# Kernel optimization log

Measured on AMD Instinct MI355X. Metric: run time of the kernel, lower is better.

The kernel has to match this reference:

```python
import jax, jax.numpy as jnp
import numpy as np
import math

B, L, E, H, D = 2, 2048, 2048, 16, 128
LOGIT_SCALE_MAX = math.log(1.0 / 0.01)
EPS = 1e-6


def rms_norm(x, scale, eps=EPS):
    # UIOLayerNorm: no mean subtraction, no bias, fp32 internals
    x32 = x.astype(jnp.float32)
    ms = jnp.mean(x32 * x32, axis=-1, keepdims=True)
    return (scale * (x32 * jax.lax.rsqrt(ms + eps)).astype(x.dtype)).astype(x.dtype)


def apply_rotary(x, rope):
    # x: [b, l, h, d]; rope: [b, l, d] interpreted as (cos, sin) interleaved pairs
    b, l, h, d = x.shape
    xr = x.astype(jnp.float32).reshape(b, l, h, d // 2, 2)
    rc = rope.astype(jnp.float32).reshape(b, l, 1, d // 2, 2)
    out = jnp.stack(
        [xr[..., 0] * rc[..., 0] - xr[..., 1] * rc[..., 1],
         xr[..., 1] * rc[..., 0] + xr[..., 0] * rc[..., 1]], axis=-1)
    return out.reshape(b, l, h, d).astype(x.dtype)


def l2_normalize(x, eps=1e-12):
    # matches F.normalize(dim=-1): x / max(||x||, eps)
    n = jnp.sqrt(jnp.sum(x * x, axis=-1, keepdims=True))
    return x / jnp.maximum(n, eps)


def setup_inputs() -> dict:
    key = jax.random.key(0)
    ks = jax.random.split(key, 12)
    scale = 1.0 / math.sqrt(E)
    return {
        "inputs_q": jax.random.normal(ks[0], (B, L, E), jnp.float32),
        "inputs_kv": jax.random.normal(ks[1], (B, L, E), jnp.float32),
        "bias": jax.random.normal(ks[2], (1, 1, L, L), jnp.float32),
        "q_sinusoids": jax.random.uniform(ks[3], (B, L, D), jnp.float32, -1.0, 1.0),
        "k_sinusoids": jax.random.uniform(ks[4], (B, L, D), jnp.float32, -1.0, 1.0),
        "Wq": jax.random.normal(ks[5], (E, E), jnp.float32) * scale,
        "Wk": jax.random.normal(ks[6], (E, E), jnp.float32) * scale,
        "Wv": jax.random.normal(ks[7], (E, E), jnp.float32) * scale,
        "Wo": jax.random.normal(ks[8], (E, E), jnp.float32) * scale,
        "q_norm_scale": jnp.ones((D,), jnp.float32),
        "k_norm_scale": jnp.ones((D,), jnp.float32),
        "logit_scale": jnp.full((H,), math.log(10.0), jnp.float32),
    }


def reference(inputs_q, inputs_kv, bias, q_sinusoids, k_sinusoids,
              Wq, Wk, Wv, Wo, q_norm_scale, k_norm_scale, logit_scale):
    dtype = inputs_q.dtype
    b, ql, e = inputs_q.shape
    kl = inputs_kv.shape[1]
    # QKV projections (nn.Linear, no bias), split heads -> [b, len, h, d]
    q = (inputs_q @ Wq.T).reshape(b, ql, H, D)
    k = (inputs_kv @ Wk.T).reshape(b, kl, H, D)
    v = (inputs_kv @ Wv.T).reshape(b, kl, H, D)
    # qk_norm (UIO RMS norm over head_dim)
    q = rms_norm(q, q_norm_scale)
    k = rms_norm(k, k_norm_scale)
    # RoPE
    q = apply_rotary(q, q_sinusoids)
    k = apply_rotary(k, k_sinusoids)
    # float32_logits
    q32 = q.astype(jnp.float32)
    k32 = k.astype(jnp.float32)
    # scaled cosine attention: L2-normalize q,k; learned per-head logit scale
    scores = jnp.einsum("bqhd,bkhd->bhqk", l2_normalize(q32), l2_normalize(k32))
    ls = jnp.exp(jnp.minimum(logit_scale, LOGIT_SCALE_MAX))
    scores = scores * ls[None, :, None, None]
    scores = scores + bias.astype(scores.dtype)
    attn = jax.nn.softmax(scores, axis=-1).astype(dtype)
    out = jnp.einsum("bhqk,bkhd->bqhd", attn, v)
    out = out.reshape(b, ql, e)
    return out @ Wo.T
```

## Files before the change

kernel.cpp:

```cpp
#include <hip/hip_runtime.h>
#include <hip/hip_bf16.h>

#define B_ 2
#define L_ 2048
#define E_ 2048
#define H_ 16
#define D_ 128
#define M_ (B_*L_)
#define NT_ (E_/64)
#define LOGIT_SCALE_MAX_ 4.6051701859880914f
#define LOG2E_ 1.44269504088896f

typedef __bf16 bf16_t;
typedef __bf16 bf16x2 __attribute__((ext_vector_type(2)));
typedef __bf16 bf16x4 __attribute__((ext_vector_type(4)));
typedef __bf16 bf16x8 __attribute__((ext_vector_type(8)));
typedef float f32x4 __attribute__((ext_vector_type(4)));
typedef float f32x16 __attribute__((ext_vector_type(16)));

#define KS_BYTE(r, cb) ((r) * 256 + ((cb) ^ (((r) & 7) << 4)))
#define VS_BYTE(r, cb) (16384 + (r) * 128 + ((cb) ^ (((r) & 7) << 4)))

#define GEMM_FRAG_IDX(r, kk, fq) ((r) * 64 + ((((kk) * 4 + (fq)) ^ ((r) & 7)) * 8))

#define NW_ 4194304L
#define NX_ 8388608L
__global__ void cvt_all_k(const float* __restrict__ xq, const float* __restrict__ xkv,
                          const float* __restrict__ bias,
                          const float* __restrict__ wq, const float* __restrict__ wk,
                          const float* __restrict__ wv, const float* __restrict__ wo,
                          bf16_t* __restrict__ ws) {
    const long NW4 = NW_ / 4, NX4 = NX_ / 4;
    long i4 = (long)blockIdx.x * 256 + threadIdx.x;
    const float* src; long off; float scale = 1.0f;
    if (i4 < 4 * NW4) {
        long r = i4 / NW4;
        src = (r == 0) ? wq : (r == 1) ? wk : (r == 2) ? wv : wo;
        off = i4 - r * NW4;
    } else if (i4 < 5 * NW4) {
        src = bias; off = i4 - 4 * NW4; scale = LOG2E_;
    } else if (i4 < 5 * NW4 + NX4) {
        src = xq; off = i4 - 5 * NW4;
    } else {
        src = xkv; off = i4 - 5 * NW4 - NX4;
    }
    float4 v = ((const float4*)src)[off];
    bf16x4 o = { (bf16_t)(v.x * scale), (bf16_t)(v.y * scale),
                 (bf16_t)(v.z * scale), (bf16_t)(v.w * scale) };
    ((bf16x4*)ws)[i4] = o;
}

template<typename OutT, int GROUPS>
__global__ __launch_bounds__(256, 2) void gemm_pipe(
    const bf16_t* __restrict__ A0, const bf16_t* __restrict__ A1,
    const bf16_t* __restrict__ W0, OutT* __restrict__ C0) {
    __shared__ bf16_t As[2][128 * 64];
    __shared__ bf16_t Bs[2][128 * 64];
    const int tid = threadIdx.x;
    const int wid = tid >> 6, lane = tid & 63;
    int bid = blockIdx.x;
    {
        int cpx = (int)gridDim.x >> 3;
        bid = (bid & 7) * cpx + (bid >> 3);
    }
    const int g = bid >> 9;
    const int wg = bid & 511;
    const int bm = wg >> 4, bn = wg & 15;
    const long arow0 = (long)bm * 128;
    const long brow0 = (long)bn * 128;
    const int fr = lane & 15, fq = lane >> 4;
    const int srow = lane >> 3;
    const int scol = ((lane & 7) ^ srow) * 8;
    const int wm = wid >> 1, wn = wid & 1;
    const bf16_t* Ab = ((GROUPS > 1 && g > 0) ? A1 : A0) + arow0 * E_;
    const bf16_t* Wb = W0 + (long)g * E_ * E_ + brow0 * E_;
    OutT* Cg = C0 + (long)g * M_ * E_;

    f32x4 acc[4][4] = {};

    auto STAGE = [&](int kt, int p) {
        #pragma unroll
        for (int q = 0; q < 4; ++q) {
            int row = wid * 32 + q * 8 + srow;
            __builtin_amdgcn_global_load_lds(
                (const __attribute__((address_space(1))) void*)(Ab + (long)row * E_ + kt + scol),
                (__attribute__((address_space(3))) void*)(&As[p][(wid * 32 + q * 8) * 64]), 16, 0, 0);
            __builtin_amdgcn_global_load_lds(
                (const __attribute__((address_space(1))) void*)(Wb + (long)row * E_ + kt + scol),
                (__attribute__((address_space(3))) void*)(&Bs[p][(wid * 32 + q * 8) * 64]), 16, 0, 0);
        }
    };

    STAGE(0, 0);
    int p = 0;
    bf16x8 a[2][4], b[2][4];
    for (int t = 0; t < NT_ - 1; ++t) {
        STAGE((t + 1) * 64, p ^ 1);
        asm volatile("s_waitcnt vmcnt(8)" ::: "memory");
        __builtin_amdgcn_s_barrier();
        __builtin_amdgcn_sched_barrier(0);
        #pragma unroll
        for (int kk = 0; kk < 2; ++kk) {
            #pragma unroll
            for (int mi = 0; mi < 4; ++mi)
                a[kk][mi] = *(const bf16x8*)&As[p][GEMM_FRAG_IDX(wm * 64 + mi * 16 + fr, kk, fq)];
            #pragma unroll
            for (int ni = 0; ni < 4; ++ni)
                b[kk][ni] = *(const bf16x8*)&Bs[p][GEMM_FRAG_IDX(wn * 64 + ni * 16 + fr, kk, fq)];
        }
        asm volatile("s_waitcnt lgkmcnt(0)" ::: "memory");
        __builtin_amdgcn_sched_barrier(0);
        __builtin_amdgcn_s_barrier();
        __builtin_amdgcn_s_setprio(1);
        #pragma unroll
        for (int kk = 0; kk < 2; ++kk)
            #pragma unroll
            for (int mi = 0; mi < 4; ++mi)
                #pragma unroll
                for (int ni = 0; ni < 4; ++ni)
                    acc[mi][ni] = __builtin_amdgcn_mfma_f32_16x16x32_bf16(a[kk][mi], b[kk][ni], acc[mi][ni], 0, 0, 0);
        __builtin_amdgcn_s_setprio(0);
        p ^= 1;
    }
    asm volatile("s_waitcnt vmcnt(0)" ::: "memory");
    __builtin_amdgcn_s_barrier();
    __builtin_amdgcn_sched_barrier(0);
    #pragma unroll
    for (int kk = 0; kk < 2; ++kk) {
        #pragma unroll
        for (int mi = 0; mi < 4; ++mi)
            a[kk][mi] = *(const bf16x8*)&As[p][GEMM_FRAG_IDX(wm * 64 + mi * 16 + fr, kk, fq)];
        #pragma unroll
        for (int ni = 0; ni < 4; ++ni)
            b[kk][ni] = *(const bf16x8*)&Bs[p][GEMM_FRAG_IDX(wn * 64 + ni * 16 + fr, kk, fq)];
        #pragma unroll
        for (int mi = 0; mi < 4; ++mi)
            #pragma unroll
            for (int ni = 0; ni < 4; ++ni)
                acc[mi][ni] = __builtin_amdgcn_mfma_f32_16x16x32_bf16(a[kk][mi], b[kk][ni], acc[mi][ni], 0, 0, 0);
    }
    #pragma unroll
    for (int mi = 0; mi < 4; ++mi) {
        #pragma unroll
        for (int i = 0; i < 4; ++i) {
            long row = arow0 + wm * 64 + mi * 16 + fq * 4 + i;
            OutT* crow = Cg + row * E_ + brow0 + wn * 64 + fr;
            #pragma unroll
            for (int ni = 0; ni < 4; ++ni)
                crow[ni * 16] = (OutT)acc[mi][ni][i];
        }
    }
}

__global__ __launch_bounds__(256) void postproc_k(
    const bf16_t* __restrict__ Pq, const bf16_t* __restrict__ Pk,
    const float* __restrict__ qsins, const float* __restrict__ ksins,
    const float* __restrict__ qnscale, const float* __restrict__ knscale,
    bf16_t* __restrict__ outq, bf16_t* __restrict__ outk) {
    const int wid = threadIdx.x >> 6, lane = threadIdx.x & 63;
    const int half = blockIdx.x >> 14;
    const long g = (long)(blockIdx.x & 16383) * 4 + wid;
    const bf16_t* P = half ? Pk : Pq;
    const float* sins = half ? ksins : qsins;
    const float* nscale = half ? knscale : qnscale;
    bf16_t* out = half ? outk : outq;
    const int h = (int)(g % H_);
    const long bl = g / H_;
    const int b = (int)(bl / L_), l = (int)(bl % L_);
    bf16x2 xv = *(const bf16x2*)(P + g * D_ + lane * 2);
    float x0 = (float)xv[0], x1 = (float)xv[1];
    float ss = x0 * x0 + x1 * x1;
    #pragma unroll
    for (int m = 1; m < 64; m <<= 1) ss += __shfl_xor(ss, m);
    float r = rsqrtf(ss * (1.0f / 128.0f) + 1e-6f);
    float y0 = x0 * r * nscale[lane * 2];
    float y1 = x1 * r * nscale[lane * 2 + 1];
    float2 cs = *(const float2*)(sins + bl * D_ + lane * 2);
    float z0 = y0 * cs.x - y1 * cs.y;
    float z1 = y1 * cs.x + y0 * cs.y;
    float n2 = z0 * z0 + z1 * z1;
    #pragma unroll
    for (int m = 1; m < 64; m <<= 1) n2 += __shfl_xor(n2, m);
    float inv = 1.0f / fmaxf(sqrtf(n2), 1e-12f);
    bf16x2 o = { (bf16_t)(z0 * inv), (bf16_t)(z1 * inv) };
    *(bf16x2*)(out + (((long)b * H_ + h) * L_ + l) * D_ + lane * 2) = o;
}

__global__ __launch_bounds__(256) void transpose_v_k(
    const bf16_t* __restrict__ Vp, bf16_t* __restrict__ Vt) {
    __shared__ bf16_t t[64 * 64];
    const int lb = blockIdx.x;
    const int db = blockIdx.y;
    const int bh = blockIdx.z;
    const int b = bh >> 4, h = bh & 15;
    const bf16_t* src = Vp + ((long)(b * L_ + lb * 64) * H_ + h) * D_ + db * 64;
    #pragma unroll
    for (int it = 0; it < 2; ++it) {
        int i = it * 256 + threadIdx.x;
        int r = i >> 3, c8 = i & 7;
        bf16x8 v = *(const bf16x8*)(src + (long)r * H_ * D_ + c8 * 8);
        *(bf16x8*)&t[r * 64 + (c8 ^ (r >> 3)) * 8] = v;
    }
    __syncthreads();
    bf16_t* dst = Vt + ((long)(b * H_ + h) * D_ + db * 64) * L_ + lb * 64;
    #pragma unroll
    for (int it = 0; it < 2; ++it) {
        int i = it * 256 + threadIdx.x;
        int d = i >> 3, l8 = i & 7;
        bf16x8 o;
        #pragma unroll
        for (int j = 0; j < 8; ++j) {
            int l = l8 * 8 + j;
            o[j] = t[l * 64 + ((d >> 3) ^ l8) * 8 + (d & 7)];
        }
        *(bf16x8*)(dst + (long)d * L_ + l8 * 8) = o;
    }
}

__global__ __launch_bounds__(256, 2) void attn_k(
    const bf16_t* __restrict__ Qn, const bf16_t* __restrict__ Kn,
    const bf16_t* __restrict__ Vt, const bf16_t* __restrict__ biasb,
    const float* __restrict__ lsg, bf16_t* __restrict__ AO) {
    __shared__ __align__(16) unsigned char smem[34816];
    const int tid = threadIdx.x;
    const int w = tid >> 6, lane = tid & 63;
    const int lane31 = lane & 31, hi = lane >> 5;
    const int qb = blockIdx.x, bh = blockIdx.y;
    const int b = bh >> 4, h = bh & 15;
    const float lsc2 = __expf(fminf(lsg[h], LOGIT_SCALE_MAX_)) * LOG2E_;
    const int qr0 = qb * 128;
    const int qloc = w * 32 + lane31;
    const bf16_t* qrow  = Qn + (((long)b * H_ + h) * L_ + qr0 + qloc) * D_;
    const bf16_t* kbase = Kn + (((long)b * H_ + h) * L_) * D_;
    const bf16_t* vtbase = Vt + ((long)(b * H_ + h) * D_) * L_;
    const bf16_t* brow  = biasb + (long)(qr0 + qloc) * L_;

    const int ksr = tid >> 4, ksc = (tid & 15) * 8;
    const int vsr = tid >> 3, vsc = (tid & 7) * 8;

    bf16x8 qreg[8];
    #pragma unroll
    for (int kk = 0; kk < 8; ++kk)
        qreg[kk] = *(const bf16x8*)(qrow + kk * 16 + 8 * hi);

    f32x16 oacc[4] = {};
    float l_ = 0.f;

    bf16x8 kreg[4], vreg[4];
    #pragma unroll
    for (int it = 0; it < 4; ++it) {
        kreg[it] = *(const bf16x8*)(kbase + (long)(it * 16 + ksr) * D_ + ksc);
        vreg[it] = *(const bf16x8*)(vtbase + (long)(it * 32 + vsr) * L_ + vsc);
    }

    for (int kt = 0; kt < L_; kt += 64) {
        __syncthreads();
        #pragma unroll
        for (int it = 0; it < 4; ++it) {
            *(bf16x8*)(smem + KS_BYTE(it * 16 + ksr, ksc * 2)) = kreg[it];
            *(bf16x8*)(smem + VS_BYTE(it * 32 + vsr, vsc * 2)) = vreg[it];
        }
        __syncthreads();
        const int ktn = (kt + 64 < L_) ? kt + 64 : 0;
        #pragma unroll
        for (int it = 0; it < 4; ++it) {
            kreg[it] = *(const bf16x8*)(kbase + (long)(ktn + it * 16 + ksr) * D_ + ksc);
            vreg[it] = *(const bf16x8*)(vtbase + (long)(it * 32 + vsr) * L_ + ktn + vsc);
        }
        bf16x4 bb[2][4];
        #pragma unroll
        for (int f = 0; f < 2; ++f)
            #pragma unroll
            for (int rr = 0; rr < 4; ++rr)
                bb[f][rr] = *(const bf16x4*)(brow + kt + f * 32 + rr * 8 + 4 * hi);
        f32x16 sacc[2] = {};
        __builtin_amdgcn_s_setprio(1);
        #pragma unroll
        for (int kk = 0; kk < 8; ++kk) {
            bf16x8 ak0 = *(const bf16x8*)(smem + KS_BYTE(lane31,      kk * 32 + 16 * hi));
            bf16x8 ak1 = *(const bf16x8*)(smem + KS_BYTE(32 + lane31, kk * 32 + 16 * hi));
            sacc[0] = __builtin_amdgcn_mfma_f32_32x32x16_bf16(ak0, qreg[kk], sacc[0], 0, 0, 0);
            sacc[1] = __builtin_amdgcn_mfma_f32_32x32x16_bf16(ak1, qreg[kk], sacc[1], 0, 0, 0);
        }
        __builtin_amdgcn_s_setprio(0);
        float ps = 0.f;
        unsigned int wv[2][4][2];
        #pragma unroll
        for (int f = 0; f < 2; ++f)
            #pragma unroll
            for (int rr = 0; rr < 4; ++rr)
                #pragma unroll
                for (int wi = 0; wi < 2; ++wi) {
                    float pa = __builtin_amdgcn_exp2f(sacc[f][rr * 4 + wi * 2]     * lsc2 + (float)bb[f][rr][wi * 2]);
                    float pc = __builtin_amdgcn_exp2f(sacc[f][rr * 4 + wi * 2 + 1] * lsc2 + (float)bb[f][rr][wi * 2 + 1]);
                    ps += pa + pc;
                    bf16x2 t = { (bf16_t)pa, (bf16_t)pc };
                    wv[f][rr][wi] = __builtin_bit_cast(unsigned int, t);
                }
        ps += __shfl_xor(ps, 32);
        l_ += ps;
        bf16x8 pb_[4];
        #pragma unroll
        for (int kk = 0; kk < 4; ++kk) {
            const int f = kk >> 1;
            const int a2 = (kk & 1) * 2;
            unsigned int A0 = wv[f][a2][0],     A1 = wv[f][a2][1];
            unsigned int B0 = wv[f][a2 + 1][0], B1 = wv[f][a2 + 1][1];
            unsigned int own0  = hi ? B0 : A0;
            unsigned int own1  = hi ? B1 : A1;
            unsigned int send0 = hi ? A0 : B0;
            unsigned int send1 = hi ? A1 : B1;
            unsigned int recv0 = __shfl_xor(send0, 32);
            unsigned int recv1 = __shfl_xor(send1, 32);
            uint4 uu;
            uu.x = hi ? recv0 : own0;
            uu.y = hi ? recv1 : own1;
            uu.z = hi ? own0  : recv0;
            uu.w = hi ? own1  : recv1;
            pb_[kk] = __builtin_bit_cast(bf16x8, uu);
        }
        __builtin_amdgcn_s_setprio(1);
        #pragma unroll
        for (int df = 0; df < 4; ++df)
            #pragma unroll
            for (int kk = 0; kk < 4; ++kk) {
                bf16x8 av = *(const bf16x8*)(smem + VS_BYTE(df * 32 + lane31, kk * 32 + 16 * hi));
                oacc[df] = __builtin_amdgcn_mfma_f32_32x32x16_bf16(av, pb_[kk], oacc[df], 0, 0, 0);
            }
        __builtin_amdgcn_s_setprio(0);
    }
    __syncthreads();
    float inv = 1.0f / l_;
    #pragma unroll
    for (int df = 0; df < 4; ++df)
        #pragma unroll
        for (int rg = 0; rg < 16; ++rg) {
            int d = df * 32 + (rg & 3) + 8 * (rg >> 2) + 4 * hi;
            *(bf16_t*)(smem + qloc * 264 + d * 2) = (bf16_t)(oacc[df][rg] * inv);
        }
    __syncthreads();
    #pragma unroll
    for (int it = 0; it < 8; ++it) {
        int idx = it * 256 + tid;
        int row = idx >> 4, c = idx & 15;
        bf16x8 v = *(const bf16x8*)(smem + row * 264 + c * 16);
        *(bf16x8*)(AO + ((long)b * L_ + qr0 + row) * E_ + h * D_ + c * 8) = v;
    }
}

extern "C" void kernel_launch(void* const* d_in, const int* in_sizes, int n_in,
                              void* d_out, int out_size, void* d_ws, size_t ws_size,
                              hipStream_t stream) {
    const float* inputs_q  = (const float*)d_in[0];
    const float* inputs_kv = (const float*)d_in[1];
    const float* bias      = (const float*)d_in[2];
    const float* q_sin     = (const float*)d_in[3];
    const float* k_sin     = (const float*)d_in[4];
    const float* Wq        = (const float*)d_in[5];
    const float* Wk        = (const float*)d_in[6];
    const float* Wv        = (const float*)d_in[7];
    const float* Wo        = (const float*)d_in[8];
    const float* qns       = (const float*)d_in[9];
    const float* kns       = (const float*)d_in[10];
    const float* lsg       = (const float*)d_in[11];

    bf16_t* ws = (bf16_t*)d_ws;
    const long NW = NW_;
    const long NX = NX_;
    bf16_t* Wq_b   = ws;
    bf16_t* Wo_b   = ws + 3 * NW;
    bf16_t* bias_b = ws + 4 * NW;
    bf16_t* Xq     = bias_b + NW;
    bf16_t* Xkv    = Xq + NX;
    bf16_t* Qp     = Xkv + NX;
    bf16_t* Kp     = Qp + NX;
    bf16_t* Vp     = Kp + NX;
    bf16_t* Qn = Xq;
    bf16_t* Kn = Xkv;
    bf16_t* AO = Qp;
    bf16_t* Vtr = Kp;
    if (ws_size < (size_t)(5 * NW + 5 * NX) * 2) return;

    {
        long n4 = (5 * NW + 2 * NX) / 4;
        cvt_all_k<<<dim3((unsigned)(n4 / 256)), dim3(256), 0, stream>>>(
            inputs_q, inputs_kv, bias, Wq, Wk, Wv, Wo, ws);
    }

    gemm_pipe<bf16_t, 3><<<dim3(1536), dim3(256), 0, stream>>>(Xq, Xkv, Wq_b, Qp);

    postproc_k<<<dim3(32768), dim3(256), 0, stream>>>(Qp, Kp, q_sin, k_sin, qns, kns, Qn, Kn);

    transpose_v_k<<<dim3(L_ / 64, D_ / 64, B_ * H_), dim3(256), 0, stream>>>(Vp, Vtr);

    attn_k<<<dim3(L_ / 128, B_ * H_), dim3(256), 0, stream>>>(Qn, Kn, Vtr, bias_b, lsg, AO);

    gemm_pipe<float, 1><<<dim3(512), dim3(256), 0, stream>>>(AO, AO, Wo_b, (float*)d_out);
}
```

Baseline: 319.4 us.

## Double-buffer K/V shared memory in attention and merge postproc with V transpose

The attention kernel now keeps two shared-memory buffers for the K and V tiles. The next tile is written into the idle buffer after the PV MFMAs, which removes one __syncthreads per iteration. Shared memory grows from about 34 KB to 64 KB per block, which may limit how many blocks fit on a CU despite the launch bounds. Separately, the q/k norm-rotary postprocess and the V transpose are merged into one launch so one kernel launch and its tail are dropped.

Result: no change. 314.5 us (-1.6%).

```diff
diff --git a/kernel.cpp b/kernel.cpp
--- a/kernel.cpp
+++ b/kernel.cpp
@@ -18,8 +18,8 @@
 typedef float f32x4 __attribute__((ext_vector_type(4)));
 typedef float f32x16 __attribute__((ext_vector_type(16)));
 
-#define KS_BYTE(r, cb) ((r) * 256 + ((cb) ^ (((r) & 7) << 4)))
-#define VS_BYTE(r, cb) (16384 + (r) * 128 + ((cb) ^ (((r) & 7) << 4)))
+#define KSB(p, r, cb) ((p) * 32768 + (r) * 256 + ((cb) ^ (((r) & 7) << 4)))
+#define VSB(p, r, cb) ((p) * 32768 + 16384 + (r) * 128 + ((cb) ^ (((r) & 7) << 4)))
 
 #define GEMM_FRAG_IDX(r, kk, fq) ((r) * 64 + ((((kk) * 4 + (fq)) ^ ((r) & 7)) * 8))
 
@@ -152,68 +152,69 @@
     }
 }
 
-__global__ __launch_bounds__(256) void postproc_k(
+__global__ __launch_bounds__(256) void post_tv_k(
     const bf16_t* __restrict__ Pq, const bf16_t* __restrict__ Pk,
+    const bf16_t* __restrict__ Vp,
     const float* __restrict__ qsins, const float* __restrict__ ksins,
     const float* __restrict__ qnscale, const float* __restrict__ knscale,
-    bf16_t* __restrict__ outq, bf16_t* __restrict__ outk) {
-    const int wid = threadIdx.x >> 6, lane = threadIdx.x & 63;
-    const int half = blockIdx.x >> 14;
-    const long g = (long)(blockIdx.x & 16383) * 4 + wid;
-    const bf16_t* P = half ? Pk : Pq;
-    const float* sins = half ? ksins : qsins;
-    const float* nscale = half ? knscale : qnscale;
-    bf16_t* out = half ? outk : outq;
-    const int h = (int)(g % H_);
-    const long bl = g / H_;
-    const int b = (int)(bl / L_), l = (int)(bl % L_);
-    bf16x2 xv = *(const bf16x2*)(P + g * D_ + lane * 2);
-    float x0 = (float)xv[0], x1 = (float)xv[1];
-    float ss = x0 * x0 + x1 * x1;
-    #pragma unroll
-    for (int m = 1; m < 64; m <<= 1) ss += __shfl_xor(ss, m);
-    float r = rsqrtf(ss * (1.0f / 128.0f) + 1e-6f);
-    float y0 = x0 * r * nscale[lane * 2];
-    float y1 = x1 * r * nscale[lane * 2 + 1];
-    float2 cs = *(const float2*)(sins + bl * D_ + lane * 2);
-    float z0 = y0 * cs.x - y1 * cs.y;
-    float z1 = y1 * cs.x + y0 * cs.y;
-    float n2 = z0 * z0 + z1 * z1;
-    #pragma unroll
-    for (int m = 1; m < 64; m <<= 1) n2 += __shfl_xor(n2, m);
-    float inv = 1.0f / fmaxf(sqrtf(n2), 1e-12f);
-    bf16x2 o = { (bf16_t)(z0 * inv), (bf16_t)(z1 * inv) };
-    *(bf16x2*)(out + (((long)b * H_ + h) * L_ + l) * D_ + lane * 2) = o;
-}
-
-__global__ __launch_bounds__(256) void transpose_v_k(
-    const bf16_t* __restrict__ Vp, bf16_t* __restrict__ Vt) {
+    bf16_t* __restrict__ outq, bf16_t* __restrict__ outk, bf16_t* __restrict__ Vt) {
     __shared__ bf16_t t[64 * 64];
-    const int lb = blockIdx.x;
-    const int db = blockIdx.y;
-    const int bh = blockIdx.z;
-    const int b = bh >> 4, h = bh & 15;
-    const bf16_t* src = Vp + ((long)(b * L_ + lb * 64) * H_ + h) * D_ + db * 64;
-    #pragma unroll
-    for (int it = 0; it < 2; ++it) {
-        int i = it * 256 + threadIdx.x;
-        int r = i >> 3, c8 = i & 7;
-        bf16x8 v = *(const bf16x8*)(src + (long)r * H_ * D_ + c8 * 8);
-        *(bf16x8*)&t[r * 64 + (c8 ^ (r >> 3)) * 8] = v;
-    }
-    __syncthreads();
-    bf16_t* dst = Vt + ((long)(b * H_ + h) * D_ + db * 64) * L_ + lb * 64;
-    #pragma unroll
-    for (int it = 0; it < 2; ++it) {
-        int i = it * 256 + threadIdx.x;
-        int d = i >> 3, l8 = i & 7;
-        bf16x8 o;
-        #pragma unroll
-        for (int j = 0; j < 8; ++j) {
-            int l = l8 * 8 + j;
-            o[j] = t[l * 64 + ((d >> 3) ^ l8) * 8 + (d & 7)];
-        }
-        *(bf16x8*)(dst + (long)d * L_ + l8 * 8) = o;
+    if (blockIdx.x < 32768) {
+        const int wid = threadIdx.x >> 6, lane = threadIdx.x & 63;
+        const int half = blockIdx.x >> 14;
+        const long g = (long)(blockIdx.x & 16383) * 4 + wid;
+        const bf16_t* P = half ? Pk : Pq;
+        const float* sins = half ? ksins : qsins;
+        const float* nscale = half ? knscale : qnscale;
+        bf16_t* out = half ? outk : outq;
+        const int h = (int)(g % H_);
+        const long bl = g / H_;
+        const int b = (int)(bl / L_), l = (int)(bl % L_);
+        bf16x2 xv = *(const bf16x2*)(P + g * D_ + lane * 2);
+        float x0 = (float)xv[0], x1 = (float)xv[1];
+        float ss = x0 * x0 + x1 * x1;
+        #pragma unroll
+        for (int m = 1; m < 64; m <<= 1) ss += __shfl_xor(ss, m);
+        float r = rsqrtf(ss * (1.0f / 128.0f) + 1e-6f);
+        float y0 = x0 * r * nscale[lane * 2];
+        float y1 = x1 * r * nscale[lane * 2 + 1];
+        float2 cs = *(const float2*)(sins + bl * D_ + lane * 2);
+        float z0 = y0 * cs.x - y1 * cs.y;
+        float z1 = y1 * cs.x + y0 * cs.y;
+        float n2 = z0 * z0 + z1 * z1;
+        #pragma unroll
+        for (int m = 1; m < 64; m <<= 1) n2 += __shfl_xor(n2, m);
+        float inv = 1.0f / fmaxf(sqrtf(n2), 1e-12f);
+        bf16x2 o = { (bf16_t)(z0 * inv), (bf16_t)(z1 * inv) };
+        *(bf16x2*)(out + (((long)b * H_ + h) * L_ + l) * D_ + lane * 2) = o;
+    } else {
+        const int idx = blockIdx.x - 32768;
+        const int lb = idx & 31;
+        const int db = (idx >> 5) & 1;
+        const int bh = idx >> 6;
+        const int b = bh >> 4, h = bh & 15;
+        const bf16_t* src = Vp + ((long)(b * L_ + lb * 64) * H_ + h) * D_ + db * 64;
+        #pragma unroll
+        for (int it = 0; it < 2; ++it) {
+            int i = it * 256 + threadIdx.x;
+            int r = i >> 3, c8 = i & 7;
+            bf16x8 v = *(const bf16x8*)(src + (long)r * H_ * D_ + c8 * 8);
+            *(bf16x8*)&t[r * 64 + (c8 ^ (r >> 3)) * 8] = v;
+        }
+        __syncthreads();
+        bf16_t* dst = Vt + ((long)(b * H_ + h) * D_ + db * 64) * L_ + lb * 64;
+        #pragma unroll
+        for (int it = 0; it < 2; ++it) {
+            int i = it * 256 + threadIdx.x;
+            int d = i >> 3, l8 = i & 7;
+            bf16x8 o;
+            #pragma unroll
+            for (int j = 0; j < 8; ++j) {
+                int l = l8 * 8 + j;
+                o[j] = t[l * 64 + ((d >> 3) ^ l8) * 8 + (d & 7)];
+            }
+            *(bf16x8*)(dst + (long)d * L_ + l8 * 8) = o;
+        }
     }
 }
 
@@ -221,7 +222,7 @@
     const bf16_t* __restrict__ Qn, const bf16_t* __restrict__ Kn,
     const bf16_t* __restrict__ Vt, const bf16_t* __restrict__ biasb,
     const float* __restrict__ lsg, bf16_t* __restrict__ AO) {
-    __shared__ __align__(16) unsigned char smem[34816];
+    __shared__ __align__(16) unsigned char smem[65536];
     const int tid = threadIdx.x;
     const int w = tid >> 6, lane = tid & 63;
     const int lane31 = lane & 31, hi = lane >> 5;
@@ -252,14 +253,14 @@
         kreg[it] = *(const bf16x8*)(kbase + (long)(it * 16 + ksr) * D_ + ksc);
         vreg[it] = *(const bf16x8*)(vtbase + (long)(it * 32 + vsr) * L_ + vsc);
     }
+    #pragma unroll
+    for (int it = 0; it < 4; ++it) {
+        *(bf16x8*)(smem + KSB(0, it * 16 + ksr, ksc * 2)) = kreg[it];
+        *(bf16x8*)(smem + VSB(0, it * 32 + vsr, vsc * 2)) = vreg[it];
+    }
+    int p = 0;
 
     for (int kt = 0; kt < L_; kt += 64) {
-        __syncthreads();
-        #pragma unroll
-        for (int it = 0; it < 4; ++it) {
-            *(bf16x8*)(smem + KS_BYTE(it * 16 + ksr, ksc * 2)) = kreg[it];
-            *(bf16x8*)(smem + VS_BYTE(it * 32 + vsr, vsc * 2)) = vreg[it];
-        }
         __syncthreads();
         const int ktn = (kt + 64 < L_) ? kt + 64 : 0;
         #pragma unroll
@@ -277,8 +278,8 @@
         __builtin_amdgcn_s_setprio(1);
         #pragma unroll
         for (int kk = 0; kk < 8; ++kk) {
-            bf16x8 ak0 = *(const bf16x8*)(smem + KS_BYTE(lane31,      kk * 32 + 16 * hi));
-            bf16x8 ak1 = *(const bf16x8*)(smem + KS_BYTE(32 + lane31, kk * 32 + 16 * hi));
+            bf16x8 ak0 = *(const bf16x8*)(smem + KSB(p, lane31,      kk * 32 + 16 * hi));
+            bf16x8 ak1 = *(const bf16x8*)(smem + KSB(p, 32 + lane31, kk * 32 + 16 * hi));
             sacc[0] = __builtin_amdgcn_mfma_f32_32x32x16_bf16(ak0, qreg[kk], sacc[0], 0, 0, 0);
             sacc[1] = __builtin_amdgcn_mfma_f32_32x32x16_bf16(ak1, qreg[kk], sacc[1], 0, 0, 0);
         }
@@ -324,10 +325,18 @@
         for (int df = 0; df < 4; ++df)
             #pragma unroll
             for (int kk = 0; kk < 4; ++kk) {
-                bf16x8 av = *(const bf16x8*)(smem + VS_BYTE(df * 32 + lane31, kk * 32 + 16 * hi));
+                bf16x8 av = *(const bf16x8*)(smem + VSB(p, df * 32 + lane31, kk * 32 + 16 * hi));
                 oacc[df] = __builtin_amdgcn_mfma_f32_32x32x16_bf16(av, pb_[kk], oacc[df], 0, 0, 0);
             }
         __builtin_amdgcn_s_setprio(0);
+        if (kt + 64 < L_) {
+            #pragma unroll
+            for (int it = 0; it < 4; ++it) {
+                *(bf16x8*)(smem + KSB(p ^ 1, it * 16 + ksr, ksc * 2)) = kreg[it];
+                *(bf16x8*)(smem + VSB(p ^ 1, it * 32 + vsr, vsc * 2)) = vreg[it];
+            }
+        }
+        p ^= 1;
     }
     __syncthreads();
     float inv = 1.0f / l_;
@@ -389,9 +398,8 @@
 
     gemm_pipe<bf16_t, 3><<<dim3(1536), dim3(256), 0, stream>>>(Xq, Xkv, Wq_b, Qp);
 
-    postproc_k<<<dim3(32768), dim3(256), 0, stream>>>(Qp, Kp, q_sin, k_sin, qns, kns, Qn, Kn);
-
-    transpose_v_k<<<dim3(L_ / 64, D_ / 64, B_ * H_), dim3(256), 0, stream>>>(Vp, Vtr);
+    post_tv_k<<<dim3(34816), dim3(256), 0, stream>>>(
+        Qp, Kp, Vp, q_sin, k_sin, qns, kns, Qn, Kn, Vtr);
 
     attn_k<<<dim3(L_ / 128, B_ * H_), dim3(256), 0, stream>>>(Qn, Kn, Vtr, bias_b, lsg, AO);
 
```
